# Performance work log

Measured on AMD Instinct MI355X. Metric: run time of the kernel, lower is better.

## Reference

```python
import jax, jax.numpy as jnp
from jax import lax
import numpy as np


def _conv(x, w, stride=1, pad=0, reflect=True, bias=None):
    if pad:
        mode = 'reflect' if reflect else 'constant'
        x = jnp.pad(x, ((0, 0), (0, 0), (pad, pad), (pad, pad)), mode=mode)
    y = lax.conv_general_dilated(x, w, (stride, stride), 'VALID',
                                 dimension_numbers=('NCHW', 'OIHW', 'NCHW'))
    if bias is not None:
        y = y + bias[None, :, None, None]
    return y


def _relu_conv(x, w, stride=1, pad=1, bias=None):
    # SimpleConv: reflect-padded conv + ReLU
    return jax.nn.relu(_conv(x, w, stride, pad, True, bias))


def _upconv(x, w):
    # ConvTranspose2d(ks=1, stride=2, pad=0, output_padding=1) + ReLU:
    # 1x1 projection placed at even output positions, zeros elsewhere.
    z = jnp.einsum('io,bihw->bohw', w[:, :, 0, 0], x)
    b, o, h, wd = z.shape
    y = jnp.zeros((b, o, 2 * h, 2 * wd), z.dtype).at[:, :, ::2, ::2].set(z)
    return jax.nn.relu(y)


def _up_bilinear(x, factor):
    # torch UpsamplingBilinear2d => align_corners=True
    b, c, h, w = x.shape

    def grid(n_in, n_out):
        src = jnp.arange(n_out, dtype=x.dtype) * ((n_in - 1) / (n_out - 1))
        i0 = jnp.clip(jnp.floor(src).astype(jnp.int32), 0, n_in - 2)
        return i0, src - i0.astype(x.dtype)

    i0, wh = grid(h, h * factor)
    j0, ww = grid(w, w * factor)
    xr = x[:, :, i0, :] * (1 - wh)[None, None, :, None] + x[:, :, i0 + 1, :] * wh[None, None, :, None]
    return xr[:, :, :, j0] * (1 - ww) + xr[:, :, :, j0 + 1] * ww


def _correlation(xa, xb, d=20):
    # corr[b, di*K+dj, i, j] = sum_c xa_pad[b,c,i+di,j+dj] * xb[b,c,i,j]
    pad = d // 2
    K = d + 1  # 21 -> 441 offsets
    b, c, h, w = xa.shape
    xp = jnp.pad(xa, ((0, 0), (0, 0), (pad, pad), (pad, pad)))
    offs = jnp.stack(jnp.meshgrid(jnp.arange(K), jnp.arange(K), indexing='ij'), -1).reshape(-1, 2)

    def body(_, off):
        sl = lax.dynamic_slice(xp, (0, 0, off[0], off[1]), (b, c, h, w))
        return None, jnp.sum(sl * xb, axis=1)

    _, out = lax.scan(body, None, offs)  # [K*K, B, H, W]
    return jnp.transpose(out, (1, 0, 2, 3))


def _forward(im1, im2, wA1, wA2, wA3, wB1, wB2, wB3, w_redir, b_redir,
             w3_1, w4, w4_1, w5, w5_1, w6,
             wd5, wd4, wd3, wd2, wf5, wf4, wf3, wpred):
    # feature extractors
    a = _relu_conv(_relu_conv(im1, wA1, 2, 3), wA2, 2, 2)   # [B,128,H/4,W/4]
    corrA = _relu_conv(a, wA3, 2, 2)                        # [B,256,H/8,W/8]
    b2 = _relu_conv(_relu_conv(im2, wB1, 2, 3), wB2, 2, 2)
    corrB = _relu_conv(b2, wB3, 2, 2)
    corr = _correlation(corrA, corrB)                       # [B,441,H/8,W/8]
    redir = _relu_conv(corrA, w_redir, 1, 0, b_redir)       # [B,32,H/8,W/8]
    x = jnp.concatenate([corr, redir], axis=1)              # 473 ch
    # encoder
    x2 = _relu_conv(x, w3_1, 1, 1)                          # 256 @ H/8
    x3 = _relu_conv(_relu_conv(x2, w4, 2, 1), w4_1, 1, 1)   # 512 @ H/16
    x4 = _relu_conv(_relu_conv(x3, w5, 2, 1), w5_1, 1, 1)   # 512 @ H/32
    x5 = _relu_conv(x4, w6, 2, 1)                           # 1024 @ H/64
    # decoder (flow convs use zero padding, no activation)
    y = jnp.concatenate([_upconv(x5, wd5), x4], axis=1)                         # 1024 @ H/32
    flow5 = _conv(y, wf5, 1, 2, False)
    y = jnp.concatenate([_upconv(y, wd4), x3, _up_bilinear(flow5, 2)], axis=1)  # 770 @ H/16
    flow4 = _conv(y, wf4, 1, 2, False)
    y = jnp.concatenate([_upconv(y, wd3), x2, _up_bilinear(flow4, 2)], axis=1)  # 386 @ H/8
    flow3 = _conv(y, wf3, 1, 2, False)
    y = jnp.concatenate([_upconv(y, wd2), a, _up_bilinear(flow3, 2)], axis=1)   # 194 @ H/4
    pred = _conv(y, wpred, 1, 2, False)
    return _up_bilinear(pred, 4)                                                # [B,2,H,W]


def setup_inputs() -> dict:
    key = jax.random.key(0)
    B, H, W = 4, 384, 384
    shapes = {
        'wA1': (64, 3, 7, 7), 'wA2': (128, 64, 5, 5), 'wA3': (256, 128, 5, 5),
        'wB1': (64, 3, 7, 7), 'wB2': (128, 64, 5, 5), 'wB3': (256, 128, 5, 5),
        'w_redir': (32, 256, 1, 1), 'b_redir': (32,),
        'w3_1': (256, 473, 3, 3), 'w4': (512, 256, 3, 3), 'w4_1': (512, 512, 3, 3),
        'w5': (512, 512, 3, 3), 'w5_1': (512, 512, 3, 3), 'w6': (1024, 512, 3, 3),
        'wd5': (1024, 512, 1, 1), 'wd4': (1024, 256, 1, 1),
        'wd3': (770, 128, 1, 1), 'wd2': (386, 64, 1, 1),
        'wf5': (2, 1024, 5, 5), 'wf4': (2, 770, 5, 5),
        'wf3': (2, 386, 5, 5), 'wpred': (2, 194, 5, 5),
    }
    ks = jax.random.split(key, len(shapes) + 2)
    inp = {
        'im1': jax.random.normal(ks[0], (B, 3, H, W), jnp.float32),
        'im2': jax.random.normal(ks[1], (B, 3, H, W), jnp.float32),
    }
    for i, (name, shp) in enumerate(shapes.items()):
        inp[name] = jax.random.normal(ks[2 + i], shp, jnp.float32) * 0.05
    return inp


def reference(im1, im2, wA1, wA2, wA3, wB1, wB2, wB3, w_redir, b_redir,
              w3_1, w4, w4_1, w5, w5_1, w6,
              wd5, wd4, wd3, wd2, wf5, wf4, wf3, wpred):
    return _forward(im1, im2, wA1, wA2, wA3, wB1, wB2, wB3, w_redir, b_redir,
                    w3_1, w4, w4_1, w5, w5_1, w6,
                    wd5, wd4, wd3, wd2, wf5, wf4, wf3, wpred)
```

## Files before the change

kernel.cpp:

```cpp
#include <hip/hip_runtime.h>
#include <hip/hip_bf16.h>


typedef unsigned short u16;
typedef __attribute__((ext_vector_type(8))) short short8;
typedef __attribute__((ext_vector_type(4))) float f32x4;

__device__ __forceinline__ int reflect_idx(int i, int n) {
  if (i < 0) i = -i;
  if (i >= n) i = 2 * n - 2 - i;
  return i;
}

__device__ __forceinline__ u16 f2bf(float f) {
  unsigned u = __float_as_uint(f);
  u += 0x7FFFu + ((u >> 16) & 1u);
  return (u16)(u >> 16);
}
__device__ __forceinline__ float bf2f(u16 h) {
  return __uint_as_float((unsigned)h << 16);
}

typedef __attribute__((address_space(1))) const unsigned int gu32;
typedef __attribute__((address_space(3))) unsigned int lu32;
__device__ __forceinline__ void gload16(const void* g, void* l) {
  __builtin_amdgcn_global_load_lds((gu32*)g, (lu32*)l, 16, 0, 0);
}

__global__ __launch_bounds__(256) void pack_w(
    const float* __restrict__ w, u16* __restrict__ hi, u16* __restrict__ lo,
    int O, int Ci, int Cip, int KH, int KW) {
  const long K = (long)Cip * KH * KW;
  const long total = (long)O * K;
  long idx = (long)blockIdx.x * 256 + threadIdx.x;
  if (idx >= total) return;
  const int o = (int)(idx / K);
  const long k = idx - (long)o * K;
  const int q = (int)(k / Cip), ci = (int)(k - (long)q * Cip);
  const int kh = q / KW, kw = q - kh * KW;
  const float v = (ci < Ci) ? w[(((size_t)o * Ci + ci) * KH + kh) * KW + kw] : 0.f;
  const u16 h = f2bf(v);
  hi[idx] = h;
  lo[idx] = f2bf(v - bf2f(h));
}

template <int K, int OCPT>
__global__ __launch_bounds__(256) void conv_direct_nhwc(
    const float* __restrict__ in, const float* __restrict__ w,
    const float* __restrict__ bias, u16* __restrict__ outhi,
    u16* __restrict__ outlo, int Cin, int Hi, int Wi, int Ho, int Wo,
    int stride, int pad, int Cip, int Hp, int Wp, int pad2, int cb) {
  const int pix = blockIdx.x * blockDim.x + threadIdx.x;
  if (pix >= Ho * Wo) return;
  const int b = blockIdx.z;
  const int oc0 = blockIdx.y * OCPT;
  const int oy = pix / Wo, ox = pix - oy * Wo;
  const int iy0 = oy * stride - pad, ix0 = ox * stride - pad;
  int iys[K], ixs[K];
#pragma unroll
  for (int k = 0; k < K; ++k) {
    iys[k] = reflect_idx(iy0 + k, Hi);
    ixs[k] = reflect_idx(ix0 + k, Wi);
  }
  float acc[OCPT];
#pragma unroll
  for (int o = 0; o < OCPT; ++o) acc[o] = bias ? bias[oc0 + o] : 0.0f;
  const size_t hw = (size_t)Hi * Wi;
  const float* inb = in + (size_t)b * Cin * hw;
  const int wstride = Cin * K * K;
  for (int ci = 0; ci < Cin; ++ci) {
    const float* inc = inb + (size_t)ci * hw;
    const float* wc = w + (size_t)oc0 * wstride + (size_t)ci * (K * K);
#pragma unroll
    for (int kh = 0; kh < K; ++kh) {
      const float* inr = inc + iys[kh] * Wi;
#pragma unroll
      for (int kw = 0; kw < K; ++kw) {
        const float v = inr[ixs[kw]];
#pragma unroll
        for (int o = 0; o < OCPT; ++o)
          acc[o] = fmaf(wc[(size_t)o * wstride + kh * K + kw], v, acc[o]);
      }
    }
  }
  const size_t o2 = ((size_t)(b * Hp + oy + pad2) * Wp + ox + pad2) * Cip + cb + oc0;
#pragma unroll
  for (int o = 0; o < OCPT; ++o) {
    const float r = fmaxf(acc[o], 0.0f);
    const u16 h = f2bf(r);
    outhi[o2 + o] = h;
    outlo[o2 + o] = f2bf(r - bf2f(h));
  }
}

__global__ __launch_bounds__(256) void halo_fill(
    u16* __restrict__ hi, u16* __restrict__ lo,
    int H, int W, int pad, int C, int Hp, int Wp) {
  const int b = blockIdx.y;
  const long idx = (long)blockIdx.x * 256 + threadIdx.x;
  if (idx >= (long)Hp * Wp * C) return;
  const int c = (int)(idx % C);
  const int cell = (int)(idx / C);
  const int x = cell % Wp, y = cell / Wp;
  if (y >= pad && y < H + pad && x >= pad && x < W + pad) return;
  const int sy = pad + reflect_idx(y - pad, H);
  const int sx = pad + reflect_idx(x - pad, W);
  const size_t dst = ((size_t)(b * Hp + y) * Wp + x) * C + c;
  const size_t src = ((size_t)(b * Hp + sy) * Wp + sx) * C + c;
  hi[dst] = hi[src];
  lo[dst] = lo[src];
}

__global__ __launch_bounds__(256) void corr_kernel(
    const float* __restrict__ tA, const float* __restrict__ tB,
    u16* __restrict__ Xh, u16* __restrict__ Xl) {
  const int C = 256, H = 48, W = 48, HW = 2304;
  const int b = blockIdx.y;
  const int p = blockIdx.x;
  const int i = p / W, j = p - i * W;
  __shared__ float xb[256];
  xb[threadIdx.x] = tB[((size_t)b * HW + p) * C + threadIdx.x];
  __syncthreads();
  const float4* b4 = (const float4*)xb;
  for (int off = threadIdx.x; off < 441; off += 256) {
    const int di = off / 21 - 10, dj = off - (off / 21) * 21 - 10;
    const int ii = i + di, jj = j + dj;
    float acc = 0.0f;
    if (ii >= 0 && ii < H && jj >= 0 && jj < W) {
      const float4* a4 = (const float4*)(tA + ((size_t)b * HW + ii * W + jj) * C);
#pragma unroll 8
      for (int c4 = 0; c4 < 64; ++c4) {
        const float4 av = a4[c4], bv = b4[c4];
        acc += av.x * bv.x + av.y * bv.y + av.z * bv.z + av.w * bv.w;
      }
    }
    const size_t o = ((size_t)(b * 50 + i + 1) * 50 + (j + 1)) * 480 + off;
    const u16 h = f2bf(acc);
    Xh[o] = h;
    Xl[o] = f2bf(acc - bf2f(h));
  }
}

struct GemmP {
  const u16 *Ah, *Al, *Bh, *Bl;
  float *C;
  float *F;
  u16 *Nh, *Nl;
  int M, N, K, Cip, Ho, Wo, HoWo, stride, KW, Hp, Wp;
  int Hp2, Wp2, pad2;
};

__global__ __launch_bounds__(256) void gemm_conv(GemmP g) {
  const int tid = threadIdx.x;
  const int lane = tid & 63, wid = tid >> 6;
  const int wr = wid >> 1, wc = wid & 1;
  const int n0 = blockIdx.x * 128, m0 = blockIdx.y * 128;

  __shared__ __align__(16) u16 sAh[4096], sAl[4096], sBh[4096], sBl[4096];

  size_t aoff[2], boff[2];
#pragma unroll
  for (int i = 0; i < 2; ++i) {
    const int s = i * 256 + tid, gs = s >> 7, r = s & 127;
    aoff[i] = (size_t)(m0 + r) * g.K + gs * 8;
    int n = n0 + r;
    if (n >= g.N) n = g.N - 1;
    const int b = n / g.HoWo, p = n - b * g.HoWo;
    const int oy = p / g.Wo, ox = p - oy * g.Wo;
    boff[i] = ((size_t)(b * g.Hp + oy * g.stride) * g.Wp + ox * g.stride) * (size_t)g.Cip + gs * 8;
  }

  f32x4 acc[4][4];
#pragma unroll
  for (int m = 0; m < 4; ++m)
#pragma unroll
    for (int n = 0; n < 4; ++n) acc[m][n] = f32x4{0.f, 0.f, 0.f, 0.f};

  int ci0 = 0, kwc = 0, khw_off = 0;
  const int rowAdd = (g.Wp - (g.KW - 1)) * g.Cip;
  for (int k0 = 0; k0 < g.K; k0 += 32) {
    const size_t ka = (size_t)k0;
    const size_t kb = (size_t)khw_off + ci0;
    __syncthreads();
#pragma unroll
    for (int i = 0; i < 2; ++i) {
      const int lo_ = (i * 256 + wid * 64) * 8;
      gload16(g.Ah + aoff[i] + ka, &sAh[lo_]);
      gload16(g.Al + aoff[i] + ka, &sAl[lo_]);
      gload16(g.Bh + boff[i] + kb, &sBh[lo_]);
      gload16(g.Bl + boff[i] + kb, &sBl[lo_]);
    }
    __syncthreads();

    const int fr = lane & 15, fs = (lane >> 4) * 128;
    short8 ah[4], al[4], bh[4], bl[4];
#pragma unroll
    for (int m = 0; m < 4; ++m) {
      const int ra = (fs + wr * 64 + m * 16 + fr) * 8;
      ah[m] = *(const short8*)&sAh[ra];
      al[m] = *(const short8*)&sAl[ra];
      const int rb = (fs + wc * 64 + m * 16 + fr) * 8;
      bh[m] = *(const short8*)&sBh[rb];
      bl[m] = *(const short8*)&sBl[rb];
    }
#pragma unroll
    for (int m = 0; m < 4; ++m)
#pragma unroll
      for (int n = 0; n < 4; ++n) {
        acc[m][n] = __builtin_amdgcn_mfma_f32_16x16x32_bf16(ah[m], bh[n], acc[m][n], 0, 0, 0);
        acc[m][n] = __builtin_amdgcn_mfma_f32_16x16x32_bf16(ah[m], bl[n], acc[m][n], 0, 0, 0);
        acc[m][n] = __builtin_amdgcn_mfma_f32_16x16x32_bf16(al[m], bh[n], acc[m][n], 0, 0, 0);
      }
    ci0 += 32;
    if (ci0 >= g.Cip) {
      ci0 = 0;
      ++kwc;
      if (kwc == g.KW) { kwc = 0; khw_off += rowAdd; }
      else khw_off += g.Cip;
    }
  }

  const int colL = lane & 15, rg = (lane >> 4) * 4;
#pragma unroll
  for (int n = 0; n < 4; ++n) {
    const int np = n0 + wc * 64 + n * 16 + colL;
    if (np >= g.N) continue;
    const int b = np / g.HoWo, p = np - b * g.HoWo;
    const int oy = p / g.Wo, ox = p - oy * g.Wo;
#pragma unroll
    for (int m = 0; m < 4; ++m) {
      const int oc0 = m0 + wr * 64 + m * 16 + rg;
      float vv[4];
#pragma unroll
      for (int j = 0; j < 4; ++j) vv[j] = fmaxf(acc[m][n][j], 0.0f);
      if (g.C) {
        const size_t base = ((size_t)b * g.M + oc0) * g.HoWo + p;
#pragma unroll
        for (int j = 0; j < 4; ++j) g.C[base + (size_t)j * g.HoWo] = vv[j];
      }
      if (g.F) {
        float4 f4 = {vv[0], vv[1], vv[2], vv[3]};
        *(float4*)&g.F[((size_t)b * g.HoWo + p) * g.M + oc0] = f4;
      }
      if (g.Nh) {
        const size_t a2 =
            ((size_t)(b * g.Hp2 + oy + g.pad2) * g.Wp2 + ox + g.pad2) * (size_t)g.M + oc0;
        ushort4 h4, l4;
        h4.x = f2bf(vv[0]); h4.y = f2bf(vv[1]); h4.z = f2bf(vv[2]); h4.w = f2bf(vv[3]);
        l4.x = f2bf(vv[0] - bf2f(h4.x)); l4.y = f2bf(vv[1] - bf2f(h4.y));
        l4.z = f2bf(vv[2] - bf2f(h4.z)); l4.w = f2bf(vv[3] - bf2f(h4.w));
        *(ushort4*)&g.Nh[a2] = h4;
        *(ushort4*)&g.Nl[a2] = l4;
      }
    }
  }
}

__global__ __launch_bounds__(256) void upconv_kernel(
    const float* __restrict__ x, const float* __restrict__ w,
    float* __restrict__ y, int Cin, int Cout, int H, int W, int Ctot, int cb) {
  const int b = blockIdx.y;
  const int hw = H * W;
  const int total = Cout * hw;
  const int idx = blockIdx.x * blockDim.x + threadIdx.x;
  if (idx >= total) return;
  const int oc = idx / hw;
  const int p = idx - oc * hw;
  const int h = p / W, wx = p - h * W;
  const float* xb = x + (size_t)b * Cin * hw + p;
  float acc = 0.0f;
  for (int ci = 0; ci < Cin; ++ci)
    acc = fmaf(xb[(size_t)ci * hw], w[(size_t)ci * Cout + oc], acc);
  const float r = fmaxf(acc, 0.0f);
  const int Wo = 2 * W;
  float* yp = y + (((size_t)b * Ctot + cb + oc) * (2 * H) + 2 * h) * Wo + 2 * wx;
  yp[0] = r; yp[1] = 0.0f; yp[Wo] = 0.0f; yp[Wo + 1] = 0.0f;
}

__global__ __launch_bounds__(256) void copy_ch(
    const float* __restrict__ src, float* __restrict__ dst,
    int Cs, int HW, int Ctot, int cb) {
  const int b = blockIdx.y;
  const int total = Cs * HW;
  for (int idx = blockIdx.x * blockDim.x + threadIdx.x; idx < total;
       idx += gridDim.x * blockDim.x) {
    const int c = idx / HW, p = idx - (idx / HW) * HW;
    dst[((size_t)b * Ctot + cb + c) * HW + p] = src[((size_t)b * Cs + c) * HW + p];
  }
}

__global__ __launch_bounds__(256) void upsample_bilinear(
    const float* __restrict__ in, float* __restrict__ out,
    int C, int Hi, int Wi, int Ho, int Wo, int Ctot, int cb) {
  const int b = blockIdx.y;
  const int total = C * Ho * Wo;
  const float sh = (float)(Hi - 1) / (float)(Ho - 1);
  const float sw = (float)(Wi - 1) / (float)(Wo - 1);
  for (int idx = blockIdx.x * blockDim.x + threadIdx.x; idx < total;
       idx += gridDim.x * blockDim.x) {
    const int c = idx / (Ho * Wo);
    const int p = idx - c * (Ho * Wo);
    const int oy = p / Wo, ox = p - oy * Wo;
    const float fy = oy * sh, fx = ox * sw;
    int y0 = (int)fy; if (y0 > Hi - 2) y0 = Hi - 2;
    int x0 = (int)fx; if (x0 > Wi - 2) x0 = Wi - 2;
    const float wy = fy - y0, wx = fx - x0;
    const float* ib = in + ((size_t)b * C + c) * Hi * Wi;
    const float v00 = ib[y0 * Wi + x0], v01 = ib[y0 * Wi + x0 + 1];
    const float v10 = ib[(y0 + 1) * Wi + x0], v11 = ib[(y0 + 1) * Wi + x0 + 1];
    const float r0 = v00 * (1.0f - wy) + v10 * wy;
    const float r1 = v01 * (1.0f - wy) + v11 * wy;
    out[((size_t)b * Ctot + cb + c) * Ho * Wo + p] = r0 * (1.0f - wx) + r1 * wx;
  }
}

__global__ __launch_bounds__(256) void conv5_splitk(
    const float* __restrict__ in, const float* __restrict__ w,
    float* __restrict__ out, int Cin, int Hi, int Wi, int cChunk) {
  const int b = blockIdx.z;
  const int c0 = blockIdx.y * cChunk;
  const int c1 = min(c0 + cChunk, Cin);
  const int pix = blockIdx.x * blockDim.x + threadIdx.x;
  if (pix >= Hi * Wi) return;
  const int oy = pix / Wi, ox = pix - oy * Wi;
  float acc0 = 0.0f, acc1 = 0.0f;
  const size_t hw = (size_t)Hi * Wi;
  for (int ci = c0; ci < c1; ++ci) {
    const float* inc = in + ((size_t)b * Cin + ci) * hw;
    const float* wc0 = w + (size_t)ci * 25;
    const float* wc1 = w + ((size_t)Cin + ci) * 25;
#pragma unroll
    for (int kh = 0; kh < 5; ++kh) {
      const int iy = oy - 2 + kh;
      if (iy < 0 || iy >= Hi) continue;
#pragma unroll
      for (int kw = 0; kw < 5; ++kw) {
        const int ix = ox - 2 + kw;
        if (ix < 0 || ix >= Wi) continue;
        const float v = inc[iy * Wi + ix];
        acc0 = fmaf(wc0[kh * 5 + kw], v, acc0);
        acc1 = fmaf(wc1[kh * 5 + kw], v, acc1);
      }
    }
  }
  const size_t o = (size_t)b * 2 * hw + pix;
  atomicAdd(&out[o], acc0);
  atomicAdd(&out[o + hw], acc1);
}

static inline int cdiv(int a, int b) { return (a + b - 1) / b; }

extern "C" void kernel_launch(void* const* d_in, const int* in_sizes, int n_in,
                              void* d_out, int out_size, void* d_ws, size_t ws_size,
                              hipStream_t stream) {
  (void)in_sizes; (void)n_in; (void)out_size; (void)ws_size;
  const float* im1     = (const float*)d_in[0];
  const float* im2     = (const float*)d_in[1];
  const float* wA1     = (const float*)d_in[2];
  const float* wA2     = (const float*)d_in[3];
  const float* wA3     = (const float*)d_in[4];
  const float* wB1     = (const float*)d_in[5];
  const float* wB2     = (const float*)d_in[6];
  const float* wB3     = (const float*)d_in[7];
  const float* w_redir = (const float*)d_in[8];
  const float* b_redir = (const float*)d_in[9];
  const float* w3_1    = (const float*)d_in[10];
  const float* w4      = (const float*)d_in[11];
  const float* w4_1    = (const float*)d_in[12];
  const float* w5      = (const float*)d_in[13];
  const float* w5_1    = (const float*)d_in[14];
  const float* w6      = (const float*)d_in[15];
  const float* wd5     = (const float*)d_in[16];
  const float* wd4     = (const float*)d_in[17];
  const float* wd3     = (const float*)d_in[18];
  const float* wd2     = (const float*)d_in[19];
  const float* wf5     = (const float*)d_in[20];
  const float* wf4     = (const float*)d_in[21];
  const float* wf3     = (const float*)d_in[22];
  const float* wpred   = (const float*)d_in[23];

  char* wsb = (char*)d_ws;
  auto at = [&](size_t byte_off) -> void* { return wsb + byte_off; };
  const int B = 4;

  u16* T1h = (u16*)at(0);               u16* T1l = (u16*)at(19668992);
  u16* C2h = (u16*)at(39337984);        u16* C2l = (u16*)at(49577984);
  float* TA    = (float*)at(59817984);
  float* TB    = (float*)at(69255168);
  float* CORRA = (float*)at(78692352);
  u16* Xh  = (u16*)at(88129536);        u16* Xl  = (u16*)at(97729536);
  u16* X2h = (u16*)at(107329536);       u16* X2l = (u16*)at(112449536);
  u16* T3h = (u16*)at(117569536);       u16* T3l = (u16*)at(120338432);
  u16* X3h = (u16*)at(123107328);       u16* X3l = (u16*)at(125876224);
  u16* T4h = (u16*)at(128645120);       u16* T4l = (u16*)at(129447936);
  u16* X4h = (u16*)at(130250752);       u16* X4l = (u16*)at(131053568);
  float* A   = (float*)at(131856384);
  float* X2f = (float*)at(150730752);
  float* X3f = (float*)at(160167936);
  float* X4f = (float*)at(164886528);
  float* X5f = (float*)at(166066176);
  u16* w2Ahp = (u16*)at(166656000);     u16* w2Alp = (u16*)at(167065600);
  u16* w2Bhp = (u16*)at(167475200);     u16* w2Blp = (u16*)at(167884800);
  u16* w3Ahp = (u16*)at(168294400);     u16* w3Alp = (u16*)at(169932800);
  u16* w3Bhp = (u16*)at(171571200);     u16* w3Blp = (u16*)at(173209600);
  u16* w31hp = (u16*)at(174848000);     u16* w31lp = (u16*)at(177059840);
  u16* w4hp  = (u16*)at(179271680);     u16* w4lp  = (u16*)at(181630976);
  u16* w41hp = (u16*)at(0);             u16* w41lp = (u16*)at(4718592);
  u16* w5hp  = (u16*)at(9437184);       u16* w5lp  = (u16*)at(14155776);
  u16* w51hp = (u16*)at(18874368);      u16* w51lp = (u16*)at(23592960);
  u16* w6hp  = (u16*)at(39337984);      u16* w6lp  = (u16*)at(48775168);
  float* Y5   = (float*)at(59817984);
  float* F5   = (float*)at(62177280);
  float* Y4   = (float*)at(62182144);
  float* F4   = (float*)at(69278464);
  float* Y3   = (float*)at(69297152);
  float* F3   = (float*)at(83526656);
  float* Y2   = (float*)at(83600384);
  float* PRED = (float*)at(112206848);

  auto pack = [&](const float* w, u16* hi, u16* lo, int O, int Ci, int Cip,
                  int KH, int KW) {
    long total = (long)O * Cip * KH * KW;
    pack_w<<<dim3((unsigned)((total + 255) / 256)), 256, 0, stream>>>(
        w, hi, lo, O, Ci, Cip, KH, KW);
  };
  auto halo = [&](u16* hi, u16* lo, int H, int W, int pad, int C, int Hp, int Wp) {
    long total = (long)Hp * Wp * C;
    halo_fill<<<dim3((unsigned)((total + 255) / 256), B), 256, 0, stream>>>(
        hi, lo, H, W, pad, C, Hp, Wp);
  };

  pack(wA2, w2Ahp, w2Alp, 128, 64, 64, 5, 5);
  pack(wB2, w2Bhp, w2Blp, 128, 64, 64, 5, 5);
  pack(wA3, w3Ahp, w3Alp, 256, 128, 128, 5, 5);
  pack(wB3, w3Bhp, w3Blp, 256, 128, 128, 5, 5);
  pack(w3_1, w31hp, w31lp, 256, 473, 480, 3, 3);
  pack(w4, w4hp, w4lp, 512, 256, 256, 3, 3);

  { dim3 g(cdiv(192 * 192, 256), 8, B);
    conv_direct_nhwc<7, 8><<<g, 256, 0, stream>>>(
        im1, wA1, nullptr, T1h, T1l, 3, 384, 384, 192, 192, 2, 3,
        64, 196, 196, 2, 0); }
  halo(T1h, T1l, 192, 192, 2, 64, 196, 196);
  { GemmP P{};
    P.Ah = w2Ahp; P.Al = w2Alp; P.Bh = T1h; P.Bl = T1l;
    P.C = A; P.Nh = C2h; P.Nl = C2l;
    P.M = 128; P.N = B * 96 * 96; P.K = 1600; P.Cip = 64;
    P.Ho = 96; P.Wo = 96; P.HoWo = 9216; P.stride = 2; P.KW = 5;
    P.Hp = 196; P.Wp = 196; P.Hp2 = 100; P.Wp2 = 100; P.pad2 = 2;
    gemm_conv<<<dim3(288, 1), 256, 0, stream>>>(P); }
  halo(C2h, C2l, 96, 96, 2, 128, 100, 100);
  { GemmP P{};
    P.Ah = w3Ahp; P.Al = w3Alp; P.Bh = C2h; P.Bl = C2l;
    P.C = CORRA; P.F = TA;
    P.M = 256; P.N = B * 48 * 48; P.K = 3200; P.Cip = 128;
    P.Ho = 48; P.Wo = 48; P.HoWo = 2304; P.stride = 2; P.KW = 5;
    P.Hp = 100; P.Wp = 100;
    gemm_conv<<<dim3(72, 2), 256, 0, stream>>>(P); }

  { dim3 g(cdiv(192 * 192, 256), 8, B);
    conv_direct_nhwc<7, 8><<<g, 256, 0, stream>>>(
        im2, wB1, nullptr, T1h, T1l, 3, 384, 384, 192, 192, 2, 3,
        64, 196, 196, 2, 0); }
  halo(T1h, T1l, 192, 192, 2, 64, 196, 196);
  { GemmP P{};
    P.Ah = w2Bhp; P.Al = w2Blp; P.Bh = T1h; P.Bl = T1l;
    P.Nh = C2h; P.Nl = C2l;
    P.M = 128; P.N = B * 96 * 96; P.K = 1600; P.Cip = 64;
    P.Ho = 96; P.Wo = 96; P.HoWo = 9216; P.stride = 2; P.KW = 5;
    P.Hp = 196; P.Wp = 196; P.Hp2 = 100; P.Wp2 = 100; P.pad2 = 2;
    gemm_conv<<<dim3(288, 1), 256, 0, stream>>>(P); }
  halo(C2h, C2l, 96, 96, 2, 128, 100, 100);
  { GemmP P{};
    P.Ah = w3Bhp; P.Al = w3Blp; P.Bh = C2h; P.Bl = C2l;
    P.F = TB;
    P.M = 256; P.N = B * 48 * 48; P.K = 3200; P.Cip = 128;
    P.Ho = 48; P.Wo = 48; P.HoWo = 2304; P.stride = 2; P.KW = 5;
    P.Hp = 100; P.Wp = 100;
    gemm_conv<<<dim3(72, 2), 256, 0, stream>>>(P); }

  pack(w4_1, w41hp, w41lp, 512, 512, 512, 3, 3);
  pack(w5, w5hp, w5lp, 512, 512, 512, 3, 3);
  pack(w5_1, w51hp, w51lp, 512, 512, 512, 3, 3);
  pack(w6, w6hp, w6lp, 1024, 512, 512, 3, 3);

  { dim3 g(cdiv(48 * 48, 256), 4, B);
    conv_direct_nhwc<1, 8><<<g, 256, 0, stream>>>(
        CORRA, w_redir, b_redir, Xh, Xl, 256, 48, 48, 48, 48, 1, 0,
        480, 50, 50, 1, 441); }
  { dim3 g(2304, B);
    corr_kernel<<<g, 256, 0, stream>>>(TA, TB, Xh, Xl); }
  halo(Xh, Xl, 48, 48, 1, 480, 50, 50);

  { GemmP P{};
    P.Ah = w31hp; P.Al = w31lp; P.Bh = Xh; P.Bl = Xl;
    P.C = X2f; P.Nh = X2h; P.Nl = X2l;
    P.M = 256; P.N = 9216; P.K = 4320; P.Cip = 480;
    P.Ho = 48; P.Wo = 48; P.HoWo = 2304; P.stride = 1; P.KW = 3;
    P.Hp = 50; P.Wp = 50; P.Hp2 = 50; P.Wp2 = 50; P.pad2 = 1;
    gemm_conv<<<dim3(72, 2), 256, 0, stream>>>(P); }
  halo(X2h, X2l, 48, 48, 1, 256, 50, 50);
  { GemmP P{};
    P.Ah = w4hp; P.Al = w4lp; P.Bh = X2h; P.Bl = X2l;
    P.Nh = T3h; P.Nl = T3l;
    P.M = 512; P.N = 2304; P.K = 2304; P.Cip = 256;
    P.Ho = 24; P.Wo = 24; P.HoWo = 576; P.stride = 2; P.KW = 3;
    P.Hp = 50; P.Wp = 50; P.Hp2 = 26; P.Wp2 = 26; P.pad2 = 1;
    gemm_conv<<<dim3(18, 4), 256, 0, stream>>>(P); }
  halo(T3h, T3l, 24, 24, 1, 512, 26, 26);
  { GemmP P{};
    P.Ah = w41hp; P.Al = w41lp; P.Bh = T3h; P.Bl = T3l;
    P.C = X3f; P.Nh = X3h; P.Nl = X3l;
    P.M = 512; P.N = 2304; P.K = 4608; P.Cip = 512;
    P.Ho = 24; P.Wo = 24; P.HoWo = 576; P.stride = 1; P.KW = 3;
    P.Hp = 26; P.Wp = 26; P.Hp2 = 26; P.Wp2 = 26; P.pad2 = 1;
    gemm_conv<<<dim3(18, 4), 256, 0, stream>>>(P); }
  halo(X3h, X3l, 24, 24, 1, 512, 26, 26);
  { GemmP P{};
    P.Ah = w5hp; P.Al = w5lp; P.Bh = X3h; P.Bl = X3l;
    P.Nh = T4h; P.Nl = T4l;
    P.M = 512; P.N = 576; P.K = 4608; P.Cip = 512;
    P.Ho = 12; P.Wo = 12; P.HoWo = 144; P.stride = 2; P.KW = 3;
    P.Hp = 26; P.Wp = 26; P.Hp2 = 14; P.Wp2 = 14; P.pad2 = 1;
    gemm_conv<<<dim3(5, 4), 256, 0, stream>>>(P); }
  halo(T4h, T4l, 12, 12, 1, 512, 14, 14);
  { GemmP P{};
    P.Ah = w51hp; P.Al = w51lp; P.Bh = T4h; P.Bl = T4l;
    P.C = X4f; P.Nh = X4h; P.Nl = X4l;
    P.M = 512; P.N = 576; P.K = 4608; P.Cip = 512;
    P.Ho = 12; P.Wo = 12; P.HoWo = 144; P.stride = 1; P.KW = 3;
    P.Hp = 14; P.Wp = 14; P.Hp2 = 14; P.Wp2 = 14; P.pad2 = 1;
    gemm_conv<<<dim3(5, 4), 256, 0, stream>>>(P); }
  halo(X4h, X4l, 12, 12, 1, 512, 14, 14);
  { GemmP P{};
    P.Ah = w6hp; P.Al = w6lp; P.Bh = X4h; P.Bl = X4l;
    P.C = X5f;
    P.M = 1024; P.N = 144; P.K = 4608; P.Cip = 512;
    P.Ho = 6; P.Wo = 6; P.HoWo = 36; P.stride = 2; P.KW = 3;
    P.Hp = 14; P.Wp = 14;
    gemm_conv<<<dim3(2, 8), 256, 0, stream>>>(P); }

  { dim3 g(cdiv(512 * 36, 256), B);  upconv_kernel<<<g, 256, 0, stream>>>(X5f, wd5, Y5, 1024, 512, 6, 6, 1024, 0); }
  { dim3 g(cdiv(512 * 144, 256), B); copy_ch<<<g, 256, 0, stream>>>(X4f, Y5, 512, 144, 1024, 512); }
  hipMemsetAsync(F5, 0, 1152 * sizeof(float), stream);
  { dim3 g(cdiv(144, 64), cdiv(1024, 64), B); conv5_splitk<<<g, 64, 0, stream>>>(Y5, wf5, F5, 1024, 12, 12, 64); }

  { dim3 g(cdiv(256 * 144, 256), B); upconv_kernel<<<g, 256, 0, stream>>>(Y5, wd4, Y4, 1024, 256, 12, 12, 770, 0); }
  { dim3 g(cdiv(512 * 576, 256), B); copy_ch<<<g, 256, 0, stream>>>(X3f, Y4, 512, 576, 770, 256); }
  { dim3 g(cdiv(2 * 576, 256), B);   upsample_bilinear<<<g, 256, 0, stream>>>(F5, Y4, 2, 12, 12, 24, 24, 770, 768); }
  hipMemsetAsync(F4, 0, 4608 * sizeof(float), stream);
  { dim3 g(cdiv(576, 64), cdiv(770, 64), B); conv5_splitk<<<g, 64, 0, stream>>>(Y4, wf4, F4, 770, 24, 24, 64); }

  { dim3 g(cdiv(128 * 576, 256), B);  upconv_kernel<<<g, 256, 0, stream>>>(Y4, wd3, Y3, 770, 128, 24, 24, 386, 0); }
  { dim3 g(cdiv(256 * 2304, 256), B); copy_ch<<<g, 256, 0, stream>>>(X2f, Y3, 256, 2304, 386, 128); }
  { dim3 g(cdiv(2 * 2304, 256), B);   upsample_bilinear<<<g, 256, 0, stream>>>(F4, Y3, 2, 24, 24, 48, 48, 386, 384); }
  hipMemsetAsync(F3, 0, 18432 * sizeof(float), stream);
  { dim3 g(cdiv(2304, 256), cdiv(386, 64), B); conv5_splitk<<<g, 256, 0, stream>>>(Y3, wf3, F3, 386, 48, 48, 64); }

  { dim3 g(cdiv(64 * 2304, 256), B);  upconv_kernel<<<g, 256, 0, stream>>>(Y3, wd2, Y2, 386, 64, 48, 48, 194, 0); }
  { dim3 g(cdiv(128 * 9216, 256), B); copy_ch<<<g, 256, 0, stream>>>(A, Y2, 128, 9216, 194, 64); }
  { dim3 g(cdiv(2 * 9216, 256), B);   upsample_bilinear<<<g, 256, 0, stream>>>(F3, Y2, 2, 48, 48, 96, 96, 194, 192); }
  hipMemsetAsync(PRED, 0, 73728 * sizeof(float), stream);
  { dim3 g(cdiv(9216, 256), cdiv(194, 64), B); conv5_splitk<<<g, 256, 0, stream>>>(Y2, wpred, PRED, 194, 96, 96, 64); }

  { dim3 g(cdiv(2 * 384 * 384, 256), B);
    upsample_bilinear<<<g, 256, 0, stream>>>(PRED, (float*)d_out, 2, 96, 96, 384, 384, 2, 0); }
}
```

Before: 4.960 ms.

## Tile correlation over 4x4 pixel blocks and template GEMM tile size for small layers

The correlation kernel now gives each block a 4x4 output tile. Each thread loads one neighbour feature vector once and dots it against 16 cached query vectors, so global reads of tA are reused across pixels instead of repeated per pixel. The GEMM conv kernel is templated on tile size, and the deep, small-N layers use 64x64 tiles to launch more blocks and fill the GPU. The first direct conv switches to 16 output channels per block. Costs are more registers per thread in the correlation kernel and less per-block reuse in the smaller GEMM tiles.

```diff
diff --git a/kernel.cpp b/kernel.cpp
--- a/kernel.cpp
+++ b/kernel.cpp
@@ -114,30 +114,55 @@
 __global__ __launch_bounds__(256) void corr_kernel(
     const float* __restrict__ tA, const float* __restrict__ tB,
     u16* __restrict__ Xh, u16* __restrict__ Xl) {
-  const int C = 256, H = 48, W = 48, HW = 2304;
+  const int W = 48, HW = 2304;
   const int b = blockIdx.y;
-  const int p = blockIdx.x;
-  const int i = p / W, j = p - i * W;
-  __shared__ float xb[256];
-  xb[threadIdx.x] = tB[((size_t)b * HW + p) * C + threadIdx.x];
+  const int tile = blockIdx.x;
+  const int i0 = (tile / 12) * 4, j0 = (tile % 12) * 4;
+  __shared__ float sB[16 * 256];
+  for (int f = threadIdx.x; f < 1024; f += 256) {
+    const int p = f >> 6, c4 = f & 63;
+    const int pi = p >> 2, pj = p & 3;
+    *(float4*)&sB[p * 256 + c4 * 4] =
+        *(const float4*)&tB[((size_t)b * HW + (i0 + pi) * W + j0 + pj) * 256 + c4 * 4];
+  }
   __syncthreads();
-  const float4* b4 = (const float4*)xb;
-  for (int off = threadIdx.x; off < 441; off += 256) {
-    const int di = off / 21 - 10, dj = off - (off / 21) * 21 - 10;
-    const int ii = i + di, jj = j + dj;
-    float acc = 0.0f;
-    if (ii >= 0 && ii < H && jj >= 0 && jj < W) {
-      const float4* a4 = (const float4*)(tA + ((size_t)b * HW + ii * W + jj) * C);
-#pragma unroll 8
+  const float4* sB4 = (const float4*)sB;
+  for (int s = threadIdx.x; s < 576; s += 256) {
+    const int ri = s / 24, rj = s - ri * 24;
+    const int gi = i0 - 10 + ri, gj = j0 - 10 + rj;
+    float acc[16];
+#pragma unroll
+    for (int p = 0; p < 16; ++p) acc[p] = 0.f;
+    if (gi >= 0 && gi < 48 && gj >= 0 && gj < 48) {
+      const float4* a4 = (const float4*)&tA[((size_t)b * HW + gi * W + gj) * 256];
+#pragma unroll 4
       for (int c4 = 0; c4 < 64; ++c4) {
-        const float4 av = a4[c4], bv = b4[c4];
-        acc += av.x * bv.x + av.y * bv.y + av.z * bv.z + av.w * bv.w;
-      }
-    }
-    const size_t o = ((size_t)(b * 50 + i + 1) * 50 + (j + 1)) * 480 + off;
-    const u16 h = f2bf(acc);
-    Xh[o] = h;
-    Xl[o] = f2bf(acc - bf2f(h));
+        const float4 av = a4[c4];
+#pragma unroll
+        for (int p = 0; p < 16; ++p) {
+          const float4 bv = sB4[p * 64 + c4];
+          acc[p] = fmaf(av.x, bv.x,
+                   fmaf(av.y, bv.y, fmaf(av.z, bv.z, fmaf(av.w, bv.w, acc[p]))));
+        }
+      }
+    }
+#pragma unroll
+    for (int pi = 0; pi < 4; ++pi) {
+      const int di = ri - 10 - pi;
+      if (di < -10 || di > 10) continue;
+#pragma unroll
+      for (int pj = 0; pj < 4; ++pj) {
+        const int dj = rj - 10 - pj;
+        if (dj < -10 || dj > 10) continue;
+        const int off = (di + 10) * 21 + (dj + 10);
+        const float v = acc[pi * 4 + pj];
+        const size_t o =
+            ((size_t)(b * 50 + i0 + pi + 1) * 50 + (j0 + pj + 1)) * 480 + off;
+        const u16 h = f2bf(v);
+        Xh[o] = h;
+        Xl[o] = f2bf(v - bf2f(h));
+      }
+    }
   }
 }
 
@@ -150,18 +175,22 @@
   int Hp2, Wp2, pad2;
 };
 
+template <int T>
 __global__ __launch_bounds__(256) void gemm_conv(GemmP g) {
+  constexpr int NF = T / 32;
+  constexpr int NL = T / 64;
+  constexpr int HALF = T / 2;
   const int tid = threadIdx.x;
   const int lane = tid & 63, wid = tid >> 6;
   const int wr = wid >> 1, wc = wid & 1;
-  const int n0 = blockIdx.x * 128, m0 = blockIdx.y * 128;
-
-  __shared__ __align__(16) u16 sAh[4096], sAl[4096], sBh[4096], sBl[4096];
-
-  size_t aoff[2], boff[2];
-#pragma unroll
-  for (int i = 0; i < 2; ++i) {
-    const int s = i * 256 + tid, gs = s >> 7, r = s & 127;
+  const int n0 = blockIdx.x * T, m0 = blockIdx.y * T;
+
+  __shared__ __align__(16) u16 sAh[T * 32], sAl[T * 32], sBh[T * 32], sBl[T * 32];
+
+  size_t aoff[NL], boff[NL];
+#pragma unroll
+  for (int i = 0; i < NL; ++i) {
+    const int s = i * 256 + tid, gs = s / T, r = s % T;
     aoff[i] = (size_t)(m0 + r) * g.K + gs * 8;
     int n = n0 + r;
     if (n >= g.N) n = g.N - 1;
@@ -170,11 +199,11 @@
     boff[i] = ((size_t)(b * g.Hp + oy * g.stride) * g.Wp + ox * g.stride) * (size_t)g.Cip + gs * 8;
   }
 
-  f32x4 acc[4][4];
-#pragma unroll
-  for (int m = 0; m < 4; ++m)
-#pragma unroll
-    for (int n = 0; n < 4; ++n) acc[m][n] = f32x4{0.f, 0.f, 0.f, 0.f};
+  f32x4 acc[NF][NF];
+#pragma unroll
+  for (int m = 0; m < NF; ++m)
+#pragma unroll
+    for (int n = 0; n < NF; ++n) acc[m][n] = f32x4{0.f, 0.f, 0.f, 0.f};
 
   int ci0 = 0, kwc = 0, khw_off = 0;
   const int rowAdd = (g.Wp - (g.KW - 1)) * g.Cip;
@@ -183,7 +212,7 @@
     const size_t kb = (size_t)khw_off + ci0;
     __syncthreads();
 #pragma unroll
-    for (int i = 0; i < 2; ++i) {
+    for (int i = 0; i < NL; ++i) {
       const int lo_ = (i * 256 + wid * 64) * 8;
       gload16(g.Ah + aoff[i] + ka, &sAh[lo_]);
       gload16(g.Al + aoff[i] + ka, &sAl[lo_]);
@@ -192,21 +221,21 @@
     }
     __syncthreads();
 
-    const int fr = lane & 15, fs = (lane >> 4) * 128;
-    short8 ah[4], al[4], bh[4], bl[4];
-#pragma unroll
-    for (int m = 0; m < 4; ++m) {
-      const int ra = (fs + wr * 64 + m * 16 + fr) * 8;
+    const int fr = lane & 15, fs = (lane >> 4) * T;
+    short8 ah[NF], al[NF], bh[NF], bl[NF];
+#pragma unroll
+    for (int m = 0; m < NF; ++m) {
+      const int ra = (fs + wr * HALF + m * 16 + fr) * 8;
       ah[m] = *(const short8*)&sAh[ra];
       al[m] = *(const short8*)&sAl[ra];
-      const int rb = (fs + wc * 64 + m * 16 + fr) * 8;
+      const int rb = (fs + wc * HALF + m * 16 + fr) * 8;
       bh[m] = *(const short8*)&sBh[rb];
       bl[m] = *(const short8*)&sBl[rb];
     }
 #pragma unroll
-    for (int m = 0; m < 4; ++m)
-#pragma unroll
-      for (int n = 0; n < 4; ++n) {
+    for (int m = 0; m < NF; ++m)
+#pragma unroll
+      for (int n = 0; n < NF; ++n) {
         acc[m][n] = __builtin_amdgcn_mfma_f32_16x16x32_bf16(ah[m], bh[n], acc[m][n], 0, 0, 0);
         acc[m][n] = __builtin_amdgcn_mfma_f32_16x16x32_bf16(ah[m], bl[n], acc[m][n], 0, 0, 0);
         acc[m][n] = __builtin_amdgcn_mfma_f32_16x16x32_bf16(al[m], bh[n], acc[m][n], 0, 0, 0);
@@ -222,14 +251,14 @@
 
   const int colL = lane & 15, rg = (lane >> 4) * 4;
 #pragma unroll
-  for (int n = 0; n < 4; ++n) {
-    const int np = n0 + wc * 64 + n * 16 + colL;
+  for (int n = 0; n < NF; ++n) {
+    const int np = n0 + wc * HALF + n * 16 + colL;
     if (np >= g.N) continue;
     const int b = np / g.HoWo, p = np - b * g.HoWo;
     const int oy = p / g.Wo, ox = p - oy * g.Wo;
 #pragma unroll
-    for (int m = 0; m < 4; ++m) {
-      const int oc0 = m0 + wr * 64 + m * 16 + rg;
+    for (int m = 0; m < NF; ++m) {
+      const int oc0 = m0 + wr * HALF + m * 16 + rg;
       float vv[4];
 #pragma unroll
       for (int j = 0; j < 4; ++j) vv[j] = fmaxf(acc[m][n][j], 0.0f);
@@ -437,8 +466,8 @@
   pack(w3_1, w31hp, w31lp, 256, 473, 480, 3, 3);
   pack(w4, w4hp, w4lp, 512, 256, 256, 3, 3);
 
-  { dim3 g(cdiv(192 * 192, 256), 8, B);
-    conv_direct_nhwc<7, 8><<<g, 256, 0, stream>>>(
+  { dim3 g(cdiv(192 * 192, 256), 4, B);
+    conv_direct_nhwc<7, 16><<<g, 256, 0, stream>>>(
         im1, wA1, nullptr, T1h, T1l, 3, 384, 384, 192, 192, 2, 3,
         64, 196, 196, 2, 0); }
   halo(T1h, T1l, 192, 192, 2, 64, 196, 196);
@@ -448,7 +477,7 @@
     P.M = 128; P.N = B * 96 * 96; P.K = 1600; P.Cip = 64;
     P.Ho = 96; P.Wo = 96; P.HoWo = 9216; P.stride = 2; P.KW = 5;
     P.Hp = 196; P.Wp = 196; P.Hp2 = 100; P.Wp2 = 100; P.pad2 = 2;
-    gemm_conv<<<dim3(288, 1), 256, 0, stream>>>(P); }
+    gemm_conv<128><<<dim3(288, 1), 256, 0, stream>>>(P); }
   halo(C2h, C2l, 96, 96, 2, 128, 100, 100);
   { GemmP P{};
     P.Ah = w3Ahp; P.Al = w3Alp; P.Bh = C2h; P.Bl = C2l;
@@ -456,10 +485,10 @@
     P.M = 256; P.N = B * 48 * 48; P.K = 3200; P.Cip = 128;
     P.Ho = 48; P.Wo = 48; P.HoWo = 2304; P.stride = 2; P.KW = 5;
     P.Hp = 100; P.Wp = 100;
-    gemm_conv<<<dim3(72, 2), 256, 0, stream>>>(P); }
-
-  { dim3 g(cdiv(192 * 192, 256), 8, B);
-    conv_direct_nhwc<7, 8><<<g, 256, 0, stream>>>(
+    gemm_conv<128><<<dim3(72, 2), 256, 0, stream>>>(P); }
+
+  { dim3 g(cdiv(192 * 192, 256), 4, B);
+    conv_direct_nhwc<7, 16><<<g, 256, 0, stream>>>(
         im2, wB1, nullptr, T1h, T1l, 3, 384, 384, 192, 192, 2, 3,
         64, 196, 196, 2, 0); }
   halo(T1h, T1l, 192, 192, 2, 64, 196, 196);
@@ -469,7 +498,7 @@
     P.M = 128; P.N = B * 96 * 96; P.K = 1600; P.Cip = 64;
     P.Ho = 96; P.Wo = 96; P.HoWo = 9216; P.stride = 2; P.KW = 5;
     P.Hp = 196; P.Wp = 196; P.Hp2 = 100; P.Wp2 = 100; P.pad2 = 2;
-    gemm_conv<<<dim3(288, 1), 256, 0, stream>>>(P); }
+    gemm_conv<128><<<dim3(288, 1), 256, 0, stream>>>(P); }
   halo(C2h, C2l, 96, 96, 2, 128, 100, 100);
   { GemmP P{};
     P.Ah = w3Bhp; P.Al = w3Blp; P.Bh = C2h; P.Bl = C2l;
@@ -477,7 +506,7 @@
     P.M = 256; P.N = B * 48 * 48; P.K = 3200; P.Cip = 128;
     P.Ho = 48; P.Wo = 48; P.HoWo = 2304; P.stride = 2; P.KW = 5;
     P.Hp = 100; P.Wp = 100;
-    gemm_conv<<<dim3(72, 2), 256, 0, stream>>>(P); }
+    gemm_conv<128><<<dim3(72, 2), 256, 0, stream>>>(P); }
 
   pack(w4_1, w41hp, w41lp, 512, 512, 512, 3, 3);
   pack(w5, w5hp, w5lp, 512, 512, 512, 3, 3);
@@ -488,7 +517,7 @@
     conv_direct_nhwc<1, 8><<<g, 256, 0, stream>>>(
         CORRA, w_redir, b_redir, Xh, Xl, 256, 48, 48, 48, 48, 1, 0,
         480, 50, 50, 1, 441); }
-  { dim3 g(2304, B);
+  { dim3 g(144, B);
     corr_kernel<<<g, 256, 0, stream>>>(TA, TB, Xh, Xl); }
   halo(Xh, Xl, 48, 48, 1, 480, 50, 50);
 
@@ -498,7 +527,7 @@
     P.M = 256; P.N = 9216; P.K = 4320; P.Cip = 480;
     P.Ho = 48; P.Wo = 48; P.HoWo = 2304; P.stride = 1; P.KW = 3;
     P.Hp = 50; P.Wp = 50; P.Hp2 = 50; P.Wp2 = 50; P.pad2 = 1;
-    gemm_conv<<<dim3(72, 2), 256, 0, stream>>>(P); }
+    gemm_conv<128><<<dim3(72, 2), 256, 0, stream>>>(P); }
   halo(X2h, X2l, 48, 48, 1, 256, 50, 50);
   { GemmP P{};
     P.Ah = w4hp; P.Al = w4lp; P.Bh = X2h; P.Bl = X2l;
@@ -506,7 +535,7 @@
     P.M = 512; P.N = 2304; P.K = 2304; P.Cip = 256;
     P.Ho = 24; P.Wo = 24; P.HoWo = 576; P.stride = 2; P.KW = 3;
     P.Hp = 50; P.Wp = 50; P.Hp2 = 26; P.Wp2 = 26; P.pad2 = 1;
-    gemm_conv<<<dim3(18, 4), 256, 0, stream>>>(P); }
+    gemm_conv<64><<<dim3(36, 8), 256, 0, stream>>>(P); }
   halo(T3h, T3l, 24, 24, 1, 512, 26, 26);
   { GemmP P{};
     P.Ah = w41hp; P.Al = w41lp; P.Bh = T3h; P.Bl = T3l;
@@ -514,7 +543,7 @@
     P.M = 512; P.N = 2304; P.K = 4608; P.Cip = 512;
     P.Ho = 24; P.Wo = 24; P.HoWo = 576; P.stride = 1; P.KW = 3;
     P.Hp = 26; P.Wp = 26; P.Hp2 = 26; P.Wp2 = 26; P.pad2 = 1;
-    gemm_conv<<<dim3(18, 4), 256, 0, stream>>>(P); }
+    gemm_conv<64><<<dim3(36, 8), 256, 0, stream>>>(P); }
   halo(X3h, X3l, 24, 24, 1, 512, 26, 26);
   { GemmP P{};
     P.Ah = w5hp; P.Al = w5lp; P.Bh = X3h; P.Bl = X3l;
@@ -522,7 +551,7 @@
     P.M = 512; P.N = 576; P.K = 4608; P.Cip = 512;
     P.Ho = 12; P.Wo = 12; P.HoWo = 144; P.stride = 2; P.KW = 3;
     P.Hp = 26; P.Wp = 26; P.Hp2 = 14; P.Wp2 = 14; P.pad2 = 1;
-    gemm_conv<<<dim3(5, 4), 256, 0, stream>>>(P); }
+    gemm_conv<64><<<dim3(9, 8), 256, 0, stream>>>(P); }
   halo(T4h, T4l, 12, 12, 1, 512, 14, 14);
   { GemmP P{};
     P.Ah = w51hp; P.Al = w51lp; P.Bh = T4h; P.Bl = T4l;
@@ -530,7 +559,7 @@
     P.M = 512; P.N = 576; P.K = 4608; P.Cip = 512;
     P.Ho = 12; P.Wo = 12; P.HoWo = 144; P.stride = 1; P.KW = 3;
     P.Hp = 14; P.Wp = 14; P.Hp2 = 14; P.Wp2 = 14; P.pad2 = 1;
-    gemm_conv<<<dim3(5, 4), 256, 0, stream>>>(P); }
+    gemm_conv<64><<<dim3(9, 8), 256, 0, stream>>>(P); }
   halo(X4h, X4l, 12, 12, 1, 512, 14, 14);
   { GemmP P{};
     P.Ah = w6hp; P.Al = w6lp; P.Bh = X4h; P.Bl = X4l;
@@ -538,7 +567,7 @@
     P.M = 1024; P.N = 144; P.K = 4608; P.Cip = 512;
     P.Ho = 6; P.Wo = 6; P.HoWo = 36; P.stride = 2; P.KW = 3;
     P.Hp = 14; P.Wp = 14;
-    gemm_conv<<<dim3(2, 8), 256, 0, stream>>>(P); }
+    gemm_conv<64><<<dim3(3, 16), 256, 0, stream>>>(P); }
 
   { dim3 g(cdiv(512 * 36, 256), B);  upconv_kernel<<<g, 256, 0, stream>>>(X5f, wd5, Y5, 1024, 512, 6, 6, 1024, 0); }
   { dim3 g(cdiv(512 * 144, 256), B); copy_ch<<<g, 256, 0, stream>>>(X4f, Y5, 512, 144, 1024, 512); }
```

After: 4.193 ms. 1.18x faster.
